# Kernel tuning notes

Hardware: AMD Instinct MI355X
Metric: run time of the kernel (lower is better)

Reference implementation:

```python
import jax, jax.numpy as jnp
import numpy as np

CROSS_NUM, EXPERT_NUM, LOW_RANK = 3, 4, 64
BATCH, DIM = 32768, 512


def setup_inputs() -> dict:
    key = jax.random.key(0)
    ks = jax.random.split(key, 6)
    s = 0.05  # small init so tanh stays in its linear-ish range
    return {
        "x": jax.random.normal(ks[0], (BATCH, DIM), dtype=jnp.float32),
        "Vs": jax.random.normal(ks[1], (CROSS_NUM, EXPERT_NUM, LOW_RANK, DIM), dtype=jnp.float32) * s,
        "Cs": jax.random.normal(ks[2], (CROSS_NUM, EXPERT_NUM, LOW_RANK, LOW_RANK), dtype=jnp.float32) * s,
        "Us": jax.random.normal(ks[3], (CROSS_NUM, EXPERT_NUM, DIM, LOW_RANK), dtype=jnp.float32) * s,
        "bias": jax.random.normal(ks[4], (CROSS_NUM, DIM), dtype=jnp.float32) * s,
        "gate_w": jax.random.normal(ks[5], (DIM, EXPERT_NUM), dtype=jnp.float32) * s,
    }


def reference(x, Vs, Cs, Us, bias, gate_w):
    # x: [B, D]. The original keeps a trailing singleton axis; we drop it and
    # batch the per-expert einsum chain over the expert axis e.
    x0 = x
    x_l = x
    for i in range(CROSS_NUM):
        # gating (shared Dense(1) per expert, applied to current x_l): [B, E]
        g = x_l @ gate_w
        # low-rank expert chain, batched over experts
        v = jnp.tanh(jnp.einsum('eld,bd->bel', Vs[i], x_l))   # [B, E, low]
        c = jnp.tanh(jnp.einsum('elk,bek->bel', Cs[i], v))    # [B, E, low]
        u = jnp.einsum('edl,bel->bed', Us[i], c)              # [B, E, D]
        expert_out = (u + bias[i][None, None, :]) * x0[:, None, :]  # [B, E, D]
        # mixture combine (raw gating scores, no softmax, as in original)
        moe = jnp.einsum('bed,be->bd', expert_out, g)
        x_l = moe + x_l
    return x_l
```

## Files before the change

### kernel.cpp

```cpp
#include <hip/hip_runtime.h>
#include <hip/hip_bf16.h>


#define CROSS   3
#define ENUM    4
#define LR      64
#define ELD     256
#define DIM     512
#define BATCH   32768
#define BT      64
#define NTHR    1024

#define XL_W    520
#define Y_W     264

typedef __bf16 bf16x8 __attribute__((ext_vector_type(8)));
typedef float  f32x4  __attribute__((ext_vector_type(4)));
typedef unsigned short us;
typedef unsigned short us4 __attribute__((ext_vector_type(4)));

__device__ __forceinline__ us f2bf(float f) {
    return __builtin_bit_cast(us, (__bf16)f);
}
__device__ __forceinline__ float bf2f(us b) {
    unsigned int u = ((unsigned int)b) << 16;
    return __builtin_bit_cast(float, u);
}
__device__ __forceinline__ float tanh_fast(float x) {
    float t = __expf(2.f * x);
    return (t - 1.f) * __builtin_amdgcn_rcpf(t + 1.f);
}

#define MFMA(a, b, c) __builtin_amdgcn_mfma_f32_16x16x32_bf16(a, b, c, 0, 0, 0)

__device__ __forceinline__ void gload_lds16(const us* g, us* l) {
    __builtin_amdgcn_global_load_lds(
        (const __attribute__((address_space(1))) unsigned int*)g,
        (__attribute__((address_space(3))) unsigned int*)l, 16, 0, 0);
}

#define WAITN(n)  asm volatile("s_waitcnt vmcnt(" #n ")" ::: "memory")
#define SBAR0()   __builtin_amdgcn_sched_barrier(0)
#define LBAR() do { SBAR0(); \
    asm volatile("s_waitcnt lgkmcnt(0)" ::: "memory"); \
    __builtin_amdgcn_s_barrier(); SBAR0(); } while (0)

__global__ __launch_bounds__(64) void swz_all(
    const float* __restrict__ Vs, const float* __restrict__ Cs,
    const float* __restrict__ Us,
    us* __restrict__ Vf, us* __restrict__ Cf, us* __restrict__ Uf)
{
    int b = blockIdx.x;
    int lane = threadIdx.x;
    const float* src;
    us* dst;
    if (b < 768) {
        int i = b >> 8, t = b & 255;
        int nt = t >> 4, ks = t & 15;
        int n  = nt * 16 + (lane & 15);
        int k0 = ks * 32 + (lane >> 4) * 8;
        src = Vs + (size_t)i * ELD * DIM + (size_t)n * DIM + k0;
        dst = Vf + (size_t)i * ELD * DIM
            + ((size_t)(nt * 16 + ks) * 64 + lane) * 8;
    } else if (b < 1536) {
        int bb = b - 768;
        int i = bb >> 8, t = bb & 255;
        int nt = t >> 3, ks = t & 7;
        int n  = nt * 16 + (lane & 15);
        int k0 = ks * 32 + (lane >> 4) * 8;
        int e = k0 >> 6, l0 = k0 & 63;
        src = Us + (size_t)i * ENUM * DIM * LR
            + (size_t)e * DIM * LR + (size_t)n * LR + l0;
        dst = Uf + (size_t)i * DIM * ELD
            + ((size_t)(nt * 8 + ks) * 64 + lane) * 8;
    } else {
        int bb = b - 1536;
        int i = bb >> 5, rest = bb & 31;
        int e = rest >> 3, t = rest & 7;
        int nt = t >> 1, ks = t & 1;
        int n  = nt * 16 + (lane & 15);
        int k0 = ks * 32 + (lane >> 4) * 8;
        src = Cs + (((size_t)(i * ENUM + e) * LR + n) * LR) + k0;
        dst = Cf + (size_t)i * ENUM * LR * LR
            + ((size_t)((e * 4 + nt) * 2 + ks) * 64 + lane) * 8;
    }
    f32x4 s0 = *reinterpret_cast<const f32x4*>(src);
    f32x4 s1 = *reinterpret_cast<const f32x4*>(src + 4);
    us4 p0, p1;
    p0[0] = f2bf(s0[0]); p0[1] = f2bf(s0[1]); p0[2] = f2bf(s0[2]); p0[3] = f2bf(s0[3]);
    p1[0] = f2bf(s1[0]); p1[1] = f2bf(s1[1]); p1[2] = f2bf(s1[2]); p1[3] = f2bf(s1[3]);
    *reinterpret_cast<us4*>(dst)     = p0;
    *reinterpret_cast<us4*>(dst + 4) = p1;
}

__global__ __launch_bounds__(NTHR, 4) void dcn_fused(
    const float* __restrict__ x,
    float* __restrict__ out,
    const us* __restrict__ Vf,
    const us* __restrict__ Cf,
    const us* __restrict__ Uf,
    const float* __restrict__ gw,
    const float* __restrict__ bias)
{
    __shared__ us xl_s[BT * XL_W];
    __shared__ __align__(16) us y_s[BT * Y_W];
    __shared__ us stg_s[3 * 8192];
    __shared__ us gw_s[4 * 512];
    __shared__ __align__(16) float g_s[BT * ENUM];
    float* sc = reinterpret_cast<float*>(y_s);

    const int tid  = threadIdx.x;
    const int wave = tid >> 6, lane = tid & 63;
    const int quad = lane >> 4, nl = lane & 15;
    const int rh = wave >> 3, wc = wave & 7;
    const int rh32 = rh * 32;
    const int row0 = blockIdx.x * BT;

#define ISSUE_V(k) gload_lds16( \
    Vl + ((size_t)(wave * 16 + (k)) * 64 + lane) * 8, \
    stg_s + ((k) % 3) * 8192 + wave * 512)
#define ISSUE_U(s) gload_lds16( \
    Ul + ((size_t)(((wave >> 1) * 4 + ((s) & 1) * 2 + (wave & 1)) * 8 \
                   + ((s) >> 1)) * 64 + lane) * 8, \
    stg_s + ((s) % 3) * 8192 + wave * 512)

    #pragma unroll
    for (int it = 0; it < 8; ++it) {
        int f4 = tid + it * NTHR;
        int r = f4 >> 7, c4 = f4 & 127;
        f32x4 v = __builtin_nontemporal_load(
            reinterpret_cast<const f32x4*>(
                x + (size_t)(row0 + r) * DIM + c4 * 4));
        us4 p;
        p[0] = f2bf(v[0]); p[1] = f2bf(v[1]); p[2] = f2bf(v[2]); p[3] = f2bf(v[3]);
        *reinterpret_cast<us4*>(&xl_s[r * XL_W + c4 * 4]) = p;
    }
    #pragma unroll
    for (int j = 0; j < 2; ++j) {
        int idx = tid * 2 + j;
        int e = idx >> 9, d = idx & 511;
        gw_s[idx] = f2bf(gw[(size_t)d * ENUM + e]);
    }
    LBAR();

    unsigned int x0p[2][4][2];
    #pragma unroll
    for (int mt = 0; mt < 2; ++mt)
        #pragma unroll
        for (int nt = 0; nt < 4; ++nt) {
            int rb = rh32 + mt * 16 + quad * 4;
            int col = wc * 64 + nt * 16 + nl;
            unsigned int b0 = xl_s[(rb + 0) * XL_W + col];
            unsigned int b1 = xl_s[(rb + 1) * XL_W + col];
            unsigned int b2 = xl_s[(rb + 2) * XL_W + col];
            unsigned int b3 = xl_s[(rb + 3) * XL_W + col];
            x0p[mt][nt][0] = b0 | (b1 << 16);
            x0p[mt][nt][1] = b2 | (b3 << 16);
        }

    const int e = wc >> 1, h = wc & 1;

    #pragma unroll 1
    for (int layer = 0; layer < CROSS; ++layer) {
        const us* Vl = Vf + (size_t)layer * ELD * DIM;
        const us* Cl = Cf + (size_t)layer * ENUM * LR * LR;
        const us* Ul = Uf + (size_t)layer * DIM * ELD;
        const float* bl = bias + layer * DIM;

        bf16x8 creg[2][2];
        #pragma unroll
        for (int ks = 0; ks < 2; ++ks)
            #pragma unroll
            for (int nt = 0; nt < 2; ++nt)
                creg[ks][nt] = *reinterpret_cast<const bf16x8*>(
                    &Cl[((size_t)((e * 4 + h * 2 + nt) * 2 + ks) * 64 + lane) * 8]);
        float bias_r[4];
        #pragma unroll
        for (int nt = 0; nt < 4; ++nt)
            bias_r[nt] = bl[wc * 64 + nt * 16 + nl];

        ISSUE_V(0); ISSUE_V(1);
        LBAR();

        {
            int grow = tid >> 4, ge = (tid >> 2) & 3, gq = tid & 3;
            float gp = 0.f;
            #pragma unroll
            for (int dd = 0; dd < 16; ++dd) {
                int d0 = gq * 128 + ((dd + gq * 4) & 15) * 8;
                bf16x8 xa = *reinterpret_cast<const bf16x8*>(
                    &xl_s[grow * XL_W + d0]);
                bf16x8 wa = *reinterpret_cast<const bf16x8*>(
                    &gw_s[ge * 512 + d0]);
                #pragma unroll
                for (int j = 0; j < 8; ++j)
                    gp += (float)xa[j] * (float)wa[j];
            }
            sc[tid] = gp;
        }
        LBAR();
        if (tid < 256)
            g_s[tid] = sc[tid * 4] + sc[tid * 4 + 1]
                     + sc[tid * 4 + 2] + sc[tid * 4 + 3];

        f32x4 acc1[2][2];
        acc1[0][0] = (f32x4)0.f; acc1[0][1] = (f32x4)0.f;
        acc1[1][0] = (f32x4)0.f; acc1[1][1] = (f32x4)0.f;
        #pragma unroll
        for (int ks = 0; ks < 16; ++ks) {
            if (ks < 15) { WAITN(1); } else { WAITN(0); }
            LBAR();
            if (ks + 2 < 16) { ISSUE_V(ks + 2); }
            bf16x8 a0 = *reinterpret_cast<const bf16x8*>(
                &xl_s[(rh32 + nl) * XL_W + ks * 32 + quad * 8]);
            bf16x8 a1 = *reinterpret_cast<const bf16x8*>(
                &xl_s[(rh32 + 16 + nl) * XL_W + ks * 32 + quad * 8]);
            const us* sl = stg_s + (ks % 3) * 8192;
            #pragma unroll
            for (int nt = 0; nt < 2; ++nt) {
                bf16x8 b = *reinterpret_cast<const bf16x8*>(
                    &sl[(wc * 2 + nt) * 512 + lane * 8]);
                acc1[0][nt] = MFMA(a0, b, acc1[0][nt]);
                acc1[1][nt] = MFMA(a1, b, acc1[1][nt]);
            }
        }
        #pragma unroll
        for (int mt = 0; mt < 2; ++mt)
            #pragma unroll
            for (int r = 0; r < 4; ++r) {
                int row = rh32 + mt * 16 + quad * 4 + r;
                #pragma unroll
                for (int nt = 0; nt < 2; ++nt)
                    y_s[row * Y_W + wc * 32 + nt * 16 + nl] =
                        f2bf(tanh_fast(acc1[mt][nt][r]));
            }
        ISSUE_U(0); ISSUE_U(1);
        LBAR();

        float Gv[2][4];
        #pragma unroll
        for (int mt = 0; mt < 2; ++mt)
            #pragma unroll
            for (int r = 0; r < 4; ++r) {
                int row = rh32 + mt * 16 + quad * 4 + r;
                f32x4 g4 = *reinterpret_cast<const f32x4*>(&g_s[row * ENUM]);
                Gv[mt][r] = g4[0] + g4[1] + g4[2] + g4[3];
            }

        f32x4 acc2[2][2];
        acc2[0][0] = (f32x4)0.f; acc2[0][1] = (f32x4)0.f;
        acc2[1][0] = (f32x4)0.f; acc2[1][1] = (f32x4)0.f;
        #pragma unroll
        for (int ks = 0; ks < 2; ++ks) {
            bf16x8 a0 = *reinterpret_cast<const bf16x8*>(
                &y_s[(rh32 + nl) * Y_W + e * 64 + ks * 32 + quad * 8]);
            bf16x8 a1 = *reinterpret_cast<const bf16x8*>(
                &y_s[(rh32 + 16 + nl) * Y_W + e * 64 + ks * 32 + quad * 8]);
            #pragma unroll
            for (int nt = 0; nt < 2; ++nt) {
                acc2[0][nt] = MFMA(a0, creg[ks][nt], acc2[0][nt]);
                acc2[1][nt] = MFMA(a1, creg[ks][nt], acc2[1][nt]);
            }
        }
        LBAR();
        #pragma unroll
        for (int mt = 0; mt < 2; ++mt)
            #pragma unroll
            for (int r = 0; r < 4; ++r) {
                int row = rh32 + mt * 16 + quad * 4 + r;
                float gv = g_s[row * ENUM + e];
                #pragma unroll
                for (int nt = 0; nt < 2; ++nt)
                    y_s[row * Y_W + e * 64 + h * 32 + nt * 16 + nl] =
                        f2bf(tanh_fast(acc2[mt][nt][r]) * gv);
            }

        f32x4 acc3[2][4];
        #pragma unroll
        for (int mt = 0; mt < 2; ++mt)
            #pragma unroll
            for (int nt = 0; nt < 4; ++nt) acc3[mt][nt] = (f32x4)0.f;
        bf16x8 za0, za1;
        #pragma unroll
        for (int s = 0; s < 16; ++s) {
            if (s < 15) { WAITN(1); } else { WAITN(0); }
            LBAR();
            if (s + 2 < 16) { ISSUE_U(s + 2); }
            if ((s & 1) == 0) {
                int ks = s >> 1;
                za0 = *reinterpret_cast<const bf16x8*>(
                    &y_s[(rh32 + nl) * Y_W + ks * 32 + quad * 8]);
                za1 = *reinterpret_cast<const bf16x8*>(
                    &y_s[(rh32 + 16 + nl) * Y_W + ks * 32 + quad * 8]);
            }
            const us* sl = stg_s + (s % 3) * 8192;
            const int nb = (s & 1) * 2;
            #pragma unroll
            for (int j = 0; j < 2; ++j) {
                bf16x8 b = *reinterpret_cast<const bf16x8*>(
                    &sl[(wc * 2 + j) * 512 + lane * 8]);
                acc3[0][nb + j] = MFMA(za0, b, acc3[0][nb + j]);
                acc3[1][nb + j] = MFMA(za1, b, acc3[1][nb + j]);
            }
        }

        #pragma unroll
        for (int nt = 0; nt < 4; ++nt) {
            int col = wc * 64 + nt * 16 + nl;
            #pragma unroll
            for (int mt = 0; mt < 2; ++mt)
                #pragma unroll
                for (int r = 0; r < 4; ++r) {
                    int row = rh32 + mt * 16 + quad * 4 + r;
                    float x0v = bf2f(
                        (us)(x0p[mt][nt][r >> 1] >> ((r & 1) * 16)));
                    float xlo = bf2f(xl_s[row * XL_W + col]);
                    float res = xlo
                              + x0v * (acc3[mt][nt][r] + bias_r[nt] * Gv[mt][r]);
                    if (layer == CROSS - 1)
                        out[(size_t)(row0 + row) * DIM + col] = res;
                    else
                        xl_s[row * XL_W + col] = f2bf(res);
                }
        }
    }
#undef ISSUE_V
#undef ISSUE_U
}

extern "C" void kernel_launch(void* const* d_in, const int* in_sizes, int n_in,
                              void* d_out, int out_size, void* d_ws,
                              size_t ws_size, hipStream_t stream) {
    const float* x      = (const float*)d_in[0];
    const float* Vs     = (const float*)d_in[1];
    const float* Cs     = (const float*)d_in[2];
    const float* Us     = (const float*)d_in[3];
    const float* bias   = (const float*)d_in[4];
    const float* gate_w = (const float*)d_in[5];
    float* out = (float*)d_out;

    us* Vf = (us*)d_ws;
    us* Uf = Vf + (size_t)CROSS * ELD * DIM;
    us* Cf = Uf + (size_t)CROSS * DIM * ELD;

    swz_all<<<1632, 64, 0, stream>>>(Vs, Cs, Us, Vf, Cf, Uf);
    dcn_fused<<<BATCH / BT, NTHR, 0, stream>>>(x, out, Vf, Cf, Uf,
                                               gate_w, bias);
}
```

Before: 322.0 us.

## Deepen weight staging pipeline to six half-size stages with wave-alternating MFMA

Measured after the change: 401.2 us. 24.6% more time.

```diff
diff --git a/kernel.cpp b/kernel.cpp
--- a/kernel.cpp
+++ b/kernel.cpp
@@ -44,6 +44,14 @@
 #define LBAR() do { SBAR0(); \
     asm volatile("s_waitcnt lgkmcnt(0)" ::: "memory"); \
     __builtin_amdgcn_s_barrier(); SBAR0(); } while (0)
+
+__device__ __forceinline__ void wait_left(int left) {
+    if (left >= 4)      WAITN(4);
+    else if (left == 3) WAITN(3);
+    else if (left == 2) WAITN(2);
+    else if (left == 1) WAITN(1);
+    else                WAITN(0);
+}
 
 __global__ __launch_bounds__(64) void swz_all(
     const float* __restrict__ Vs, const float* __restrict__ Cs,
@@ -104,7 +112,7 @@
 {
     __shared__ us xl_s[BT * XL_W];
     __shared__ __align__(16) us y_s[BT * Y_W];
-    __shared__ us stg_s[3 * 8192];
+    __shared__ us stg_s[6 * 4096];
     __shared__ us gw_s[4 * 512];
     __shared__ __align__(16) float g_s[BT * ENUM];
     float* sc = reinterpret_cast<float*>(y_s);
@@ -116,21 +124,26 @@
     const int rh32 = rh * 32;
     const int row0 = blockIdx.x * BT;
 
-#define ISSUE_V(k) gload_lds16( \
-    Vl + ((size_t)(wave * 16 + (k)) * 64 + lane) * 8, \
-    stg_s + ((k) % 3) * 8192 + wave * 512)
-#define ISSUE_U(s) gload_lds16( \
-    Ul + ((size_t)(((wave >> 1) * 4 + ((s) & 1) * 2 + (wave & 1)) * 8 \
-                   + ((s) >> 1)) * 64 + lane) * 8, \
-    stg_s + ((s) % 3) * 8192 + wave * 512)
+    const int sj = wave >> 1;
+    const int sh = wave & 1;
+    const int myh1 = wc >> 2, jb1 = (wc & 3) * 2;
+    const int myq3 = wc >> 1, jb3 = (wc & 1) * 4;
+
+#define ISSUE_V(s) do { if (lane < 32) gload_lds16( \
+    Vl + ((size_t)(((((s) & 1) * 8 + sj) * 16 + ((s) >> 1)) * 64 \
+                   + sh * 32 + lane) * 8), \
+    stg_s + ((s) % 6) * 4096 + sj * 512 + sh * 256); } while (0)
+#define ISSUE_U(s) do { if (lane < 32) gload_lds16( \
+    Ul + ((size_t)(((((s) & 3) * 8 + sj) * 8 + ((s) >> 2)) * 64 \
+                   + sh * 32 + lane) * 8), \
+    stg_s + ((s) % 6) * 4096 + sj * 512 + sh * 256); } while (0)
 
     #pragma unroll
     for (int it = 0; it < 8; ++it) {
         int f4 = tid + it * NTHR;
         int r = f4 >> 7, c4 = f4 & 127;
-        f32x4 v = __builtin_nontemporal_load(
-            reinterpret_cast<const f32x4*>(
-                x + (size_t)(row0 + r) * DIM + c4 * 4));
+        f32x4 v = *reinterpret_cast<const f32x4*>(
+            x + (size_t)(row0 + r) * DIM + c4 * 4);
         us4 p;
         p[0] = f2bf(v[0]); p[1] = f2bf(v[1]); p[2] = f2bf(v[2]); p[3] = f2bf(v[3]);
         *reinterpret_cast<us4*>(&xl_s[r * XL_W + c4 * 4]) = p;
@@ -174,12 +187,8 @@
             for (int nt = 0; nt < 2; ++nt)
                 creg[ks][nt] = *reinterpret_cast<const bf16x8*>(
                     &Cl[((size_t)((e * 4 + h * 2 + nt) * 2 + ks) * 64 + lane) * 8]);
-        float bias_r[4];
-        #pragma unroll
-        for (int nt = 0; nt < 4; ++nt)
-            bias_r[nt] = bl[wc * 64 + nt * 16 + nl];
-
-        ISSUE_V(0); ISSUE_V(1);
+
+        ISSUE_V(0); ISSUE_V(1); ISSUE_V(2); ISSUE_V(3); ISSUE_V(4);
         LBAR();
 
         {
@@ -207,21 +216,24 @@
         acc1[0][0] = (f32x4)0.f; acc1[0][1] = (f32x4)0.f;
         acc1[1][0] = (f32x4)0.f; acc1[1][1] = (f32x4)0.f;
         #pragma unroll
-        for (int ks = 0; ks < 16; ++ks) {
-            if (ks < 15) { WAITN(1); } else { WAITN(0); }
+        for (int s = 0; s < 32; ++s) {
+            wait_left(31 - s);
             LBAR();
-            if (ks + 2 < 16) { ISSUE_V(ks + 2); }
-            bf16x8 a0 = *reinterpret_cast<const bf16x8*>(
-                &xl_s[(rh32 + nl) * XL_W + ks * 32 + quad * 8]);
-            bf16x8 a1 = *reinterpret_cast<const bf16x8*>(
-                &xl_s[(rh32 + 16 + nl) * XL_W + ks * 32 + quad * 8]);
-            const us* sl = stg_s + (ks % 3) * 8192;
-            #pragma unroll
-            for (int nt = 0; nt < 2; ++nt) {
-                bf16x8 b = *reinterpret_cast<const bf16x8*>(
-                    &sl[(wc * 2 + nt) * 512 + lane * 8]);
-                acc1[0][nt] = MFMA(a0, b, acc1[0][nt]);
-                acc1[1][nt] = MFMA(a1, b, acc1[1][nt]);
+            if (s + 5 < 32) { ISSUE_V(s + 5); }
+            if ((s & 1) == myh1) {
+                const int ks = s >> 1;
+                bf16x8 a0 = *reinterpret_cast<const bf16x8*>(
+                    &xl_s[(rh32 + nl) * XL_W + ks * 32 + quad * 8]);
+                bf16x8 a1 = *reinterpret_cast<const bf16x8*>(
+                    &xl_s[(rh32 + 16 + nl) * XL_W + ks * 32 + quad * 8]);
+                const us* sl = stg_s + (s % 6) * 4096;
+                #pragma unroll
+                for (int nt = 0; nt < 2; ++nt) {
+                    bf16x8 b = *reinterpret_cast<const bf16x8*>(
+                        &sl[(jb1 + nt) * 512 + lane * 8]);
+                    acc1[0][nt] = MFMA(a0, b, acc1[0][nt]);
+                    acc1[1][nt] = MFMA(a1, b, acc1[1][nt]);
+                }
             }
         }
         #pragma unroll
@@ -234,7 +246,7 @@
                     y_s[row * Y_W + wc * 32 + nt * 16 + nl] =
                         f2bf(tanh_fast(acc1[mt][nt][r]));
             }
-        ISSUE_U(0); ISSUE_U(1);
+        ISSUE_U(0); ISSUE_U(1); ISSUE_U(2); ISSUE_U(3); ISSUE_U(4);
         LBAR();
 
         float Gv[2][4];
@@ -280,29 +292,32 @@
         for (int mt = 0; mt < 2; ++mt)
             #pragma unroll
             for (int nt = 0; nt < 4; ++nt) acc3[mt][nt] = (f32x4)0.f;
-        bf16x8 za0, za1;
-        #pragma unroll
-        for (int s = 0; s < 16; ++s) {
-            if (s < 15) { WAITN(1); } else { WAITN(0); }
+        #pragma unroll
+        for (int s = 0; s < 32; ++s) {
+            wait_left(31 - s);
             LBAR();
-            if (s + 2 < 16) { ISSUE_U(s + 2); }
-            if ((s & 1) == 0) {
-                int ks = s >> 1;
-                za0 = *reinterpret_cast<const bf16x8*>(
+            if (s + 5 < 32) { ISSUE_U(s + 5); }
+            if ((s & 3) == myq3) {
+                const int ks = s >> 2;
+                bf16x8 za0 = *reinterpret_cast<const bf16x8*>(
                     &y_s[(rh32 + nl) * Y_W + ks * 32 + quad * 8]);
-                za1 = *reinterpret_cast<const bf16x8*>(
+                bf16x8 za1 = *reinterpret_cast<const bf16x8*>(
                     &y_s[(rh32 + 16 + nl) * Y_W + ks * 32 + quad * 8]);
-            }
-            const us* sl = stg_s + (s % 3) * 8192;
-            const int nb = (s & 1) * 2;
-            #pragma unroll
-            for (int j = 0; j < 2; ++j) {
-                bf16x8 b = *reinterpret_cast<const bf16x8*>(
-                    &sl[(wc * 2 + j) * 512 + lane * 8]);
-                acc3[0][nb + j] = MFMA(za0, b, acc3[0][nb + j]);
-                acc3[1][nb + j] = MFMA(za1, b, acc3[1][nb + j]);
-            }
-        }
+                const us* sl = stg_s + (s % 6) * 4096;
+                #pragma unroll
+                for (int nt = 0; nt < 4; ++nt) {
+                    bf16x8 b = *reinterpret_cast<const bf16x8*>(
+                        &sl[(jb3 + nt) * 512 + lane * 8]);
+                    acc3[0][nt] = MFMA(za0, b, acc3[0][nt]);
+                    acc3[1][nt] = MFMA(za1, b, acc3[1][nt]);
+                }
+            }
+        }
+
+        float bias_r[4];
+        #pragma unroll
+        for (int nt = 0; nt < 4; ++nt)
+            bias_r[nt] = bl[wc * 64 + nt * 16 + nl];
 
         #pragma unroll
         for (int nt = 0; nt < 4; ++nt) {
```
